# Kernel tuning notes

Hardware: AMD Instinct MI355X
Metric: run time of the kernel (lower is better)

## Reference

```python
import jax, jax.numpy as jnp
import numpy as np

IN_SIZE = 256
HID = 256          # memory_vector_size == hidd_size
MEM = 128          # memory_size
ALPHA_SIG = -0.4
GAMMA = 0.3
GATE = 1.0 / (1.0 + np.exp(-ALPHA_SIG))  # sigmoid(alpha_sig) ~ 0.4013
B, T = 128, 1024


def _l2norm(x):
    # F.normalize(x, dim=-1): x / max(||x||2, 1e-12)
    return x / jnp.maximum(jnp.linalg.norm(x, axis=-1, keepdims=True), 1e-12)


def setup_inputs() -> dict:
    key = jax.random.key(0)
    ks = jax.random.split(key, 5)
    s = 1.0 / np.sqrt(HID)  # torch LSTMCell default init range
    X = jax.random.normal(ks[0], (B, T, IN_SIZE), dtype=jnp.float32)
    W_ih = jax.random.uniform(ks[1], (4 * HID, IN_SIZE), jnp.float32, -s, s)
    W_hh = jax.random.uniform(ks[2], (4 * HID, HID), jnp.float32, -s, s)
    b_ih = jax.random.uniform(ks[3], (4 * HID,), jnp.float32, -s, s)
    b_hh = jax.random.uniform(ks[4], (4 * HID,), jnp.float32, -s, s)
    return {"X": X, "W_ih": W_ih, "W_hh": W_hh, "b_ih": b_ih, "b_hh": b_hh}


def _forward(X, W_ih, W_hh, b_ih, b_hh):
    Bt = X.shape[0]
    gate = jnp.asarray(GATE, X.dtype)
    gamma = jnp.asarray(GAMMA, X.dtype)

    def lstm_cell(x, h, c):
        z = x @ W_ih.T + b_ih + h @ W_hh.T + b_hh  # [B, 4H]
        i, f, g, o = jnp.split(z, 4, axis=-1)
        c_new = jax.nn.sigmoid(f) * c + jax.nn.sigmoid(i) * jnp.tanh(g)
        h_new = jax.nn.sigmoid(o) * jnp.tanh(c_new)
        return h_new, c_new

    def step(carry, x_t):
        h, c, M, w_u, prev_w_r = carry
        h, c = lstm_cell(x_t, h, c)
        # read head: softmax over cosine similarity with memory rows
        inner = h @ M.T                                    # [B, MEM]
        denom = (jnp.linalg.norm(h, axis=-1, keepdims=True)
                 * jnp.linalg.norm(M, axis=-1)[None, :])   # [B, MEM]
        w_r = jax.nn.softmax(inner / (denom + 1e-8), axis=-1)
        read = w_r @ M                                     # [B, H]
        out_t = jnp.concatenate([h, read], axis=-1)        # [B, 2H]
        # write (original is under torch.no_grad / detached)
        hs = jax.lax.stop_gradient(h)
        wrs = jax.lax.stop_gradient(w_r)
        w_lu = (1.0 - gate) * jax.nn.one_hot(jnp.argmin(w_u, axis=-1), MEM, dtype=M.dtype)
        w_w = gate * prev_w_r + w_lu                       # [B, MEM]
        M_new = _l2norm(M + w_w.T @ hs)                    # einsum('bi,bj->bij').sum(0) == w_w.T @ h
        w_u_new = _l2norm(gamma * w_u + wrs + w_w)
        return (h, c, M_new, w_u_new, wrs), out_t

    init = (jnp.zeros((Bt, HID), X.dtype),
            jnp.zeros((Bt, HID), X.dtype),
            jnp.zeros((MEM, HID), X.dtype),   # self.M starts as zeros
            jnp.zeros((Bt, MEM), X.dtype),    # w_u
            jnp.zeros((Bt, MEM), X.dtype))    # prev_w_r
    _, ys = jax.lax.scan(step, init, jnp.swapaxes(X, 0, 1))  # ys: [T, B, 2H]
    return jnp.swapaxes(ys, 0, 1)                            # [B, T, 2H]


def reference(X, W_ih, W_hh, b_ih, b_hh):
    return _forward(X, W_ih, W_hh, b_ih, b_hh)
```

## Files before the change

### kernel.cpp

```cpp
#include <hip/hip_runtime.h>
#include <math.h>

#define BATCH 128
#define TSTEPS 1024
#define INSZ 256
#define HSZ 256
#define MEMN 128

#define NWG_A 128
#define NWG_B 64
#define NWG_C 32
#define NWG 224
#define NTHR 256

#define GATE_C 0.40131233988754794f
#define OMG_C  (1.0f - GATE_C)
#define GAMMA_C 0.3f

__device__ float g_hT[(size_t)TSTEPS * HSZ * BATCH];
__device__ float g_M [(size_t)TSTEPS * MEMN * HSZ];
__device__ float g_Mn[(size_t)TSTEPS * MEMN];
__device__ float g_ww[(size_t)TSTEPS * BATCH * MEMN];
__device__ float g_c[BATCH * HSZ];
__device__ int g_fA[TSTEPS * NWG_A];
__device__ int g_fB[TSTEPS * NWG_B];
__device__ int g_fC[TSTEPS * NWG_C];

__global__ void reset_ctrl_kernel() {
    const int gt = blockIdx.x * 256 + threadIdx.x, gn = gridDim.x * 256;
    for (int i = gt; i < TSTEPS * NWG_A; i += gn)
        __hip_atomic_store(&g_fA[i], 0, __ATOMIC_RELAXED, __HIP_MEMORY_SCOPE_AGENT);
    for (int i = gt; i < TSTEPS * NWG_B; i += gn)
        __hip_atomic_store(&g_fB[i], 0, __ATOMIC_RELAXED, __HIP_MEMORY_SCOPE_AGENT);
    for (int i = gt; i < TSTEPS * NWG_C; i += gn)
        __hip_atomic_store(&g_fC[i], 0, __ATOMIC_RELAXED, __HIP_MEMORY_SCOPE_AGENT);
}

__device__ __forceinline__ float sigf(float x) { return 1.0f / (1.0f + expf(-x)); }

__device__ __forceinline__ void st_wt(float* p, float v) {
    __hip_atomic_store(p, v, __ATOMIC_RELAXED, __HIP_MEMORY_SCOPE_AGENT);
}
__device__ __forceinline__ void st_flag(int* p, int v) {
    __hip_atomic_store(p, v, __ATOMIC_RELAXED, __HIP_MEMORY_SCOPE_AGENT);
}
__device__ __forceinline__ void wait_vm0() { asm volatile("s_waitcnt vmcnt(0)" ::: "memory"); }

__device__ __forceinline__ void wait_flags(int* f, int n, int want, int lane) {
    int it = 0;
    for (;;) {
        bool ok = true;
        for (int i = lane; i < n; i += 64)
            ok &= (__hip_atomic_load(&f[i], __ATOMIC_RELAXED, __HIP_MEMORY_SCOPE_AGENT) == want);
        if (__all(ok)) break;
        __builtin_amdgcn_s_sleep(1);
        if (++it > (1 << 22)) break;
    }
}

__global__ void __launch_bounds__(NTHR, 1)
mann_persist(const float* __restrict__ X, const float* __restrict__ Wih,
             const float* __restrict__ Whh, const float* __restrict__ bih,
             const float* __restrict__ bhh, float* __restrict__ out) {
    __shared__ float4 s_x4[64 * 128];
    __shared__ float s_aux[4096];
    __shared__ float s_red8[8];
    __shared__ unsigned long long s_redu8[8];

    const int w = blockIdx.x, tid = threadIdx.x;
    const int lane = tid & 63, wv = tid >> 6;

    auto red256sum = [&](float v) -> float {
#pragma unroll
        for (int o = 32; o; o >>= 1) v += __shfl_xor(v, o, 64);
        if (lane == 0) s_red8[wv] = v;
        __syncthreads();
        float r = (s_red8[0] + s_red8[1]) + (s_red8[2] + s_red8[3]);
        __syncthreads();
        return r;
    };
    auto grpsum = [&](float v) -> float {
#pragma unroll
        for (int o = 32; o; o >>= 1) v += __shfl_xor(v, o, 64);
        if (lane == 0) s_red8[wv] = v;
        __syncthreads();
        float r = s_red8[(tid >> 7) * 2] + s_red8[(tid >> 7) * 2 + 1];
        __syncthreads();
        return r;
    };
    auto grpmax = [&](float v) -> float {
#pragma unroll
        for (int o = 32; o; o >>= 1) v = fmaxf(v, __shfl_xor(v, o, 64));
        if (lane == 0) s_red8[wv] = v;
        __syncthreads();
        float r = fmaxf(s_red8[(tid >> 7) * 2], s_red8[(tid >> 7) * 2 + 1]);
        __syncthreads();
        return r;
    };
    auto grpminu = [&](unsigned long long v) -> unsigned long long {
#pragma unroll
        for (int o = 32; o; o >>= 1) {
            unsigned long long o2 = __shfl_xor(v, o, 64);
            v = (o2 < v) ? o2 : v;
        }
        if (lane == 0) s_redu8[wv] = v;
        __syncthreads();
        unsigned long long a = s_redu8[(tid >> 7) * 2], b2 = s_redu8[(tid >> 7) * 2 + 1];
        unsigned long long r = (a < b2) ? a : b2;
        __syncthreads();
        return r;
    };

    if (w < NWG_A) {
        const int bb = w >> 6, jb = w & 63;
        const int bglob = bb * 64 + lane;
        float biasA[4];
#pragma unroll
        for (int g = 0; g < 4; ++g) {
            const int row = g * HSZ + jb * 4 + wv;
            biasA[g] = bih[row] + bhh[row];
        }

        auto stageX = [&](int t) {
            const int kq = tid & 63, bofs = tid >> 6;
#pragma unroll 4
            for (int rep = 0; rep < 16; ++rep) {
                const int b = rep * 4 + bofs;
                const float4 v = *(const float4*)(X + ((size_t)(bb * 64 + b) * TSTEPS + t) * INSZ + kq * 4);
                s_x4[b * 128 + (kq ^ (b & 7))] = v;
            }
        };
        auto computeRegion = [&](float (&acc)[16], const float* __restrict__ Wb, const int kofs) {
            const int kbase = kofs + wv * 64;
#pragma unroll 4
            for (int k4 = 0; k4 < 16; ++k4) {
                const int kg = kbase + k4 * 4;
                const float4 xv = s_x4[lane * 128 + ((kg >> 2) ^ (lane & 7))];
                const int kl = kg - kofs;
#pragma unroll
                for (int rr = 0; rr < 16; ++rr) {
                    const int grow = (rr >> 2) * HSZ + jb * 4 + (rr & 3);
                    const float4 wv4 = *(const float4*)(Wb + (size_t)grow * 256 + kl);
                    acc[rr] += wv4.x * xv.x + wv4.y * xv.y + wv4.z * xv.z + wv4.w * xv.w;
                }
            }
        };

        stageX(0);
        __syncthreads();

        for (int t = 0; t < TSTEPS; ++t) {
            float acc[16];
#pragma unroll
            for (int i = 0; i < 16; ++i) acc[i] = 0.f;
            float4 hv[16];
            if (t > 0) {
                if (wv == 0) wait_flags(g_fA + (size_t)(t - 1) * NWG_A, NWG_A, t, lane);
                __syncthreads();
                asm volatile("" ::: "memory");
#pragma unroll
                for (int rep = 0; rep < 16; ++rep) {
                    const int j0 = (wv * 16 + rep) * 4;
                    const size_t base = ((size_t)(t - 1) * HSZ + j0) * BATCH + bglob;
                    float4 v;
                    v.x = g_hT[base];
                    v.y = g_hT[base + BATCH];
                    v.z = g_hT[base + 2 * BATCH];
                    v.w = g_hT[base + 3 * BATCH];
                    hv[rep] = v;
                }
            }
            computeRegion(acc, Wih, 0);
            if (t > 0) {
#pragma unroll
                for (int rep = 0; rep < 16; ++rep)
                    s_x4[lane * 128 + ((64 + wv * 16 + rep) ^ (lane & 7))] = hv[rep];
            } else {
                const float4 z4 = make_float4(0.f, 0.f, 0.f, 0.f);
#pragma unroll
                for (int rep = 0; rep < 16; ++rep)
                    s_x4[lane * 128 + ((64 + wv * 16 + rep) ^ (lane & 7))] = z4;
            }
            __syncthreads();
            computeRegion(acc, Whh, 256);
#pragma unroll
            for (int rr = 0; rr < 16; ++rr) s_aux[(wv * 16 + rr) * 64 + lane] = acc[rr];
            __syncthreads();
            float z[4];
#pragma unroll
            for (int g = 0; g < 4; ++g) {
                const int rr = g * 4 + wv;
                z[g] = ((s_aux[rr * 64 + lane] + s_aux[(16 + rr) * 64 + lane]) +
                        (s_aux[(32 + rr) * 64 + lane] + s_aux[(48 + rr) * 64 + lane])) + biasA[g];
            }
            const int jglob = jb * 4 + wv;
            const int cidx = bglob * HSZ + jglob;
            const float cold = (t == 0) ? 0.f : g_c[cidx];
            const float cn = sigf(z[1]) * cold + sigf(z[0]) * tanhf(z[2]);
            const float hn = sigf(z[3]) * tanhf(cn);
            g_c[cidx] = cn;
            st_wt(&g_hT[((size_t)t * HSZ + jglob) * BATCH + bglob], hn);
            wait_vm0();
            __syncthreads();
            if (tid == 0) st_flag(&g_fA[(size_t)t * NWG_A + w], t + 1);
            if (t + 1 < TSTEPS) stageX(t + 1);
        }
    } else if (w < NWG_A + NWG_B) {
        const int bwg = w - NWG_A;
        const int grp = tid >> 7, lm = tid & 127;
        const int bB = bwg * 2 + grp;
        float* s_h2 = s_aux;
        float* s_wr2 = s_aux + 512;
        float wwreg = (lm == 0) ? OMG_C : 0.f;
        float wureg = 0.f;

        for (int t = 0; t < TSTEPS; ++t) {
            if (wv == 0) wait_flags(g_fA + (size_t)t * NWG_A, NWG_A, t + 1, lane);
            else if (wv == 1 && t > 0) wait_flags(g_fC + (size_t)(t - 1) * NWG_C, NWG_C, t, lane);
            __syncthreads();
            asm volatile("" ::: "memory");
            s_h2[grp * 256 + lm] = g_hT[((size_t)t * HSZ + lm) * BATCH + bB];
            s_h2[grp * 256 + lm + 128] = g_hT[((size_t)t * HSZ + lm + 128) * BATCH + bB];
            __syncthreads();
            const float hv0 = s_h2[grp * 256 + lm], hv1 = s_h2[grp * 256 + lm + 128];
            const float hnorm = sqrtf(grpsum(hv0 * hv0 + hv1 * hv1));
            float sc = 0.f;
            if (t > 0) {
                const float4* mrow = (const float4*)&g_M[((size_t)t * MEMN + lm) * HSZ];
                const float4* h4 = (const float4*)&s_h2[grp * 256];
                float a = 0.f;
#pragma unroll 8
                for (int c = 0; c < 64; ++c) {
                    const float4 m4 = mrow[c], x4 = h4[c];
                    a += m4.x * x4.x + m4.y * x4.y + m4.z * x4.z + m4.w * x4.w;
                }
                const float mn = g_Mn[(size_t)t * MEMN + lm];
                sc = a / (hnorm * mn + 1e-8f);
            }
            const float mx = grpmax(sc);
            const float ev = expf(sc - mx);
            const float es = grpsum(ev);
            const float wr = ev / es;
            s_wr2[grp * 128 + lm] = wr;
            __syncthreads();
            float rd0 = 0.f, rd1 = 0.f;
            if (t > 0) {
#pragma unroll 8
                for (int m = 0; m < 128; ++m) {
                    const float mv = g_M[((size_t)t * MEMN + m) * HSZ + tid];
                    rd0 += s_wr2[m] * mv;
                    rd1 += s_wr2[128 + m] * mv;
                }
            }
            const int b0 = bwg * 2, b1 = b0 + 1;
            float* o0 = out + ((size_t)b0 * TSTEPS + t) * 512;
            float* o1 = out + ((size_t)b1 * TSTEPS + t) * 512;
            o0[tid] = s_h2[tid];
            o1[tid] = s_h2[256 + tid];
            o0[256 + tid] = rd0;
            o1[256 + tid] = rd1;
            const float un = GAMMA_C * wureg + wr + wwreg;
            const float un2 = grpsum(un * un);
            const float us = 1.0f / fmaxf(sqrtf(un2), 1e-12f);
            const float wun = un * us;
            wureg = wun;
            unsigned long long key =
                (((unsigned long long)__float_as_uint(wun)) << 32) | (unsigned)lm;
            const unsigned long long mk = grpminu(key);
            const int amin = (int)(mk & 0xffffffffu);
            const float wwn = GATE_C * wr + ((lm == amin) ? OMG_C : 0.f);
            wwreg = wwn;
            if (t + 1 < TSTEPS)
                st_wt(&g_ww[((size_t)(t + 1) * BATCH + bB) * MEMN + lm], wwn);
            wait_vm0();
            __syncthreads();
            if (tid == 0) st_flag(&g_fB[(size_t)t * NWG_B + bwg], t + 1);
        }
    } else {
        const int cwg = w - NWG_A - NWG_B;
        const int m0 = cwg * 4;
        float* s_wwc = s_aux;

        for (int t = 0; t < TSTEPS - 1; ++t) {
            if (wv == 0) wait_flags(g_fA + (size_t)t * NWG_A, NWG_A, t + 1, lane);
            else if (wv == 1 && t > 0) wait_flags(g_fB + (size_t)(t - 1) * NWG_B, NWG_B, t, lane);
            __syncthreads();
            asm volatile("" ::: "memory");
#pragma unroll
            for (int e = tid; e < 512; e += 256) {
                const int mi = e & 3, b = e >> 2;
                float v;
                if (t > 0) v = g_ww[((size_t)t * BATCH + b) * MEMN + m0 + mi];
                else v = (m0 + mi == 0) ? OMG_C : 0.f;
                s_wwc[mi * 128 + b] = v;
            }
            __syncthreads();
            float macc[4];
#pragma unroll
            for (int mi = 0; mi < 4; ++mi)
                macc[mi] = (t > 0) ? g_M[((size_t)t * MEMN + m0 + mi) * HSZ + tid] : 0.f;
            const float4* ht4 = (const float4*)&g_hT[((size_t)t * HSZ + tid) * BATCH];
#pragma unroll 4
            for (int b4 = 0; b4 < 32; ++b4) {
                const float4 hv4 = ht4[b4];
#pragma unroll
                for (int mi = 0; mi < 4; ++mi) {
                    const float* wc = &s_wwc[mi * 128 + b4 * 4];
                    macc[mi] += wc[0] * hv4.x + wc[1] * hv4.y + wc[2] * hv4.z + wc[3] * hv4.w;
                }
            }
#pragma unroll
            for (int mi = 0; mi < 4; ++mi) {
                const float nrm = sqrtf(red256sum(macc[mi] * macc[mi]));
                const float scale = 1.0f / fmaxf(nrm, 1e-12f);
                const float vo = macc[mi] * scale;
                st_wt(&g_M[((size_t)(t + 1) * MEMN + m0 + mi) * HSZ + tid], vo);
                if (tid == 0) st_wt(&g_Mn[(size_t)(t + 1) * MEMN + m0 + mi], nrm * scale);
            }
            wait_vm0();
            __syncthreads();
            if (tid == 0) st_flag(&g_fC[(size_t)t * NWG_C + cwg], t + 1);
        }
    }
}

extern "C" void kernel_launch(void* const* d_in, const int* in_sizes, int n_in,
                              void* d_out, int out_size, void* d_ws, size_t ws_size,
                              hipStream_t stream) {
    const float* X   = (const float*)d_in[0];
    const float* Wih = (const float*)d_in[1];
    const float* Whh = (const float*)d_in[2];
    const float* bih = (const float*)d_in[3];
    const float* bhh = (const float*)d_in[4];
    float* out = (float*)d_out;
    (void)in_sizes; (void)n_in; (void)out_size; (void)d_ws; (void)ws_size;

    hipLaunchKernelGGL(reset_ctrl_kernel, dim3(224), dim3(256), 0, stream);
    hipLaunchKernelGGL(mann_persist, dim3(NWG), dim3(NTHR), 0, stream,
                       X, Wih, Whh, bih, bhh, out);
}
```

Measured before the change: 24.04 ms.

## Repartition LSTM workgroups by hidden unit with LDS-resident weights and batch-major h copy

The LSTM-stage workgroups now each own two hidden units across the whole batch instead of four units for half the batch. This lets their slice of W_ih/W_hh be cached in LDS once rather than re-read from global memory every timestep, and X and h are staged in double-buffered 128-wide tiles. The cell state stays in a register instead of going to global memory. A batch-major copy of h is also written so the read-head stage gets coalesced loads, and the memory-update stage keeps its M rows in registers. In exchange every LSTM group now stages the full X row for all 128 batches each step, adds extra barriers, and writes h twice.

```diff
diff --git a/kernel.cpp b/kernel.cpp
--- a/kernel.cpp
+++ b/kernel.cpp
@@ -18,10 +18,10 @@
 #define GAMMA_C 0.3f
 
 __device__ float g_hT[(size_t)TSTEPS * HSZ * BATCH];
+__device__ float g_hB[(size_t)TSTEPS * BATCH * HSZ];
 __device__ float g_M [(size_t)TSTEPS * MEMN * HSZ];
 __device__ float g_Mn[(size_t)TSTEPS * MEMN];
 __device__ float g_ww[(size_t)TSTEPS * BATCH * MEMN];
-__device__ float g_c[BATCH * HSZ];
 __device__ int g_fA[TSTEPS * NWG_A];
 __device__ int g_fB[TSTEPS * NWG_B];
 __device__ int g_fC[TSTEPS * NWG_C];
@@ -40,6 +40,11 @@
 
 __device__ __forceinline__ void st_wt(float* p, float v) {
     __hip_atomic_store(p, v, __ATOMIC_RELAXED, __HIP_MEMORY_SCOPE_AGENT);
+}
+__device__ __forceinline__ void st_wt2(float* p, float lo, float hi) {
+    unsigned long long pk = (unsigned long long)__float_as_uint(lo) |
+                            ((unsigned long long)__float_as_uint(hi) << 32);
+    __hip_atomic_store((unsigned long long*)p, pk, __ATOMIC_RELAXED, __HIP_MEMORY_SCOPE_AGENT);
 }
 __device__ __forceinline__ void st_flag(int* p, int v) {
     __hip_atomic_store(p, v, __ATOMIC_RELAXED, __HIP_MEMORY_SCOPE_AGENT);
@@ -62,13 +67,15 @@
 mann_persist(const float* __restrict__ X, const float* __restrict__ Wih,
              const float* __restrict__ Whh, const float* __restrict__ bih,
              const float* __restrict__ bhh, float* __restrict__ out) {
-    __shared__ float4 s_x4[64 * 128];
-    __shared__ float s_aux[4096];
+    __shared__ float4 s_xt[2][4096];
+    __shared__ float4 s_w[1024];
+    __shared__ float s_tr[256];
     __shared__ float s_red8[8];
     __shared__ unsigned long long s_redu8[8];
 
     const int w = blockIdx.x, tid = threadIdx.x;
     const int lane = tid & 63, wv = tid >> 6;
+    float* s_aux = (float*)s_xt;
 
     auto red256sum = [&](float v) -> float {
 #pragma unroll
@@ -112,98 +119,106 @@
     };
 
     if (w < NWG_A) {
-        const int bb = w >> 6, jb = w & 63;
-        const int bglob = bb * 64 + lane;
+        const int j2 = wv >> 1, bh = wv & 1;
+        const int bA = bh * 64 + lane;
+        const int jA = 2 * w + j2;
         float biasA[4];
 #pragma unroll
-        for (int g = 0; g < 4; ++g) {
-            const int row = g * HSZ + jb * 4 + wv;
-            biasA[g] = bih[row] + bhh[row];
-        }
-
-        auto stageX = [&](int t) {
-            const int kq = tid & 63, bofs = tid >> 6;
-#pragma unroll 4
+        for (int g = 0; g < 4; ++g) biasA[g] = bih[g * HSZ + jA] + bhh[g * HSZ + jA];
+
+#pragma unroll
+        for (int rep = 0; rep < 4; ++rep) {
+            const int id = rep * 256 + tid;
+            const int r = id >> 7, c = id & 127;
+            const int grow = (r >> 1) * HSZ + 2 * w + (r & 1);
+            float4 v;
+            if (c < 64) v = ((const float4*)(Wih + (size_t)grow * INSZ))[c];
+            else        v = ((const float4*)(Whh + (size_t)grow * HSZ))[c - 64];
+            s_w[r * 128 + c] = v;
+        }
+
+        auto stageX = [&](int t, int kt, float4* buf) {
+#pragma unroll
             for (int rep = 0; rep < 16; ++rep) {
-                const int b = rep * 4 + bofs;
-                const float4 v = *(const float4*)(X + ((size_t)(bb * 64 + b) * TSTEPS + t) * INSZ + kq * 4);
-                s_x4[b * 128 + (kq ^ (b & 7))] = v;
+                const int id = rep * 256 + tid;
+                const int b = id >> 5, c = id & 31;
+                buf[b * 32 + (c ^ (b & 7))] =
+                    *(const float4*)(X + ((size_t)b * TSTEPS + t) * INSZ + kt * 128 + c * 4);
             }
         };
-        auto computeRegion = [&](float (&acc)[16], const float* __restrict__ Wb, const int kofs) {
-            const int kbase = kofs + wv * 64;
-#pragma unroll 4
-            for (int k4 = 0; k4 < 16; ++k4) {
-                const int kg = kbase + k4 * 4;
-                const float4 xv = s_x4[lane * 128 + ((kg >> 2) ^ (lane & 7))];
-                const int kl = kg - kofs;
-#pragma unroll
-                for (int rr = 0; rr < 16; ++rr) {
-                    const int grow = (rr >> 2) * HSZ + jb * 4 + (rr & 3);
-                    const float4 wv4 = *(const float4*)(Wb + (size_t)grow * 256 + kl);
-                    acc[rr] += wv4.x * xv.x + wv4.y * xv.y + wv4.z * xv.z + wv4.w * xv.w;
+        auto loadH = [&](int tprev, int jt, float4 (&hvr)[16]) {
+#pragma unroll
+            for (int rep = 0; rep < 16; ++rep) {
+                const int id = rep * 256 + tid;
+                const int b = id >> 5, c = id & 31;
+                hvr[rep] = *(const float4*)(g_hB + ((size_t)tprev * BATCH + b) * HSZ + jt * 128 + c * 4);
+            }
+        };
+        auto writeTile = [&](float4 (&hvr)[16], float4* buf) {
+#pragma unroll
+            for (int rep = 0; rep < 16; ++rep) {
+                const int id = rep * 256 + tid;
+                const int b = id >> 5, c = id & 31;
+                buf[b * 32 + (c ^ (b & 7))] = hvr[rep];
+            }
+        };
+        auto computeTile = [&](const float4* buf, int T, float (&zacc)[4]) {
+#pragma unroll 8
+            for (int c = 0; c < 32; ++c) {
+                const float4 xv = buf[bA * 32 + (c ^ (bA & 7))];
+#pragma unroll
+                for (int g = 0; g < 4; ++g) {
+                    const float4 wv4 = s_w[(g * 2 + j2) * 128 + T * 32 + c];
+                    zacc[g] += wv4.x * xv.x + wv4.y * xv.y + wv4.z * xv.z + wv4.w * xv.w;
                 }
             }
         };
 
-        stageX(0);
-        __syncthreads();
+        stageX(0, 0, s_xt[0]);
+        stageX(0, 1, s_xt[1]);
+        __syncthreads();
+        float creg = 0.f;
 
         for (int t = 0; t < TSTEPS; ++t) {
-            float acc[16];
-#pragma unroll
-            for (int i = 0; i < 16; ++i) acc[i] = 0.f;
-            float4 hv[16];
             if (t > 0) {
                 if (wv == 0) wait_flags(g_fA + (size_t)(t - 1) * NWG_A, NWG_A, t, lane);
                 __syncthreads();
                 asm volatile("" ::: "memory");
-#pragma unroll
-                for (int rep = 0; rep < 16; ++rep) {
-                    const int j0 = (wv * 16 + rep) * 4;
-                    const size_t base = ((size_t)(t - 1) * HSZ + j0) * BATCH + bglob;
-                    float4 v;
-                    v.x = g_hT[base];
-                    v.y = g_hT[base + BATCH];
-                    v.z = g_hT[base + 2 * BATCH];
-                    v.w = g_hT[base + 3 * BATCH];
-                    hv[rep] = v;
-                }
-            }
-            computeRegion(acc, Wih, 0);
-            if (t > 0) {
-#pragma unroll
-                for (int rep = 0; rep < 16; ++rep)
-                    s_x4[lane * 128 + ((64 + wv * 16 + rep) ^ (lane & 7))] = hv[rep];
-            } else {
-                const float4 z4 = make_float4(0.f, 0.f, 0.f, 0.f);
-#pragma unroll
-                for (int rep = 0; rep < 16; ++rep)
-                    s_x4[lane * 128 + ((64 + wv * 16 + rep) ^ (lane & 7))] = z4;
-            }
-            __syncthreads();
-            computeRegion(acc, Whh, 256);
-#pragma unroll
-            for (int rr = 0; rr < 16; ++rr) s_aux[(wv * 16 + rr) * 64 + lane] = acc[rr];
-            __syncthreads();
+            }
+            float zacc[4] = {0.f, 0.f, 0.f, 0.f};
+            float4 hvr[16];
+            if (t > 0) loadH(t - 1, 0, hvr);
+            else { const float4 z4 = make_float4(0.f,0.f,0.f,0.f);
+#pragma unroll
+                   for (int r = 0; r < 16; ++r) hvr[r] = z4; }
+            computeTile(s_xt[0], 0, zacc);
+            __syncthreads();
+            writeTile(hvr, s_xt[0]);
+            if (t > 0) loadH(t - 1, 1, hvr);
+            computeTile(s_xt[1], 1, zacc);
+            __syncthreads();
+            writeTile(hvr, s_xt[1]);
+            computeTile(s_xt[0], 2, zacc);
+            __syncthreads();
+            computeTile(s_xt[1], 3, zacc);
             float z[4];
 #pragma unroll
-            for (int g = 0; g < 4; ++g) {
-                const int rr = g * 4 + wv;
-                z[g] = ((s_aux[rr * 64 + lane] + s_aux[(16 + rr) * 64 + lane]) +
-                        (s_aux[(32 + rr) * 64 + lane] + s_aux[(48 + rr) * 64 + lane])) + biasA[g];
-            }
-            const int jglob = jb * 4 + wv;
-            const int cidx = bglob * HSZ + jglob;
-            const float cold = (t == 0) ? 0.f : g_c[cidx];
-            const float cn = sigf(z[1]) * cold + sigf(z[0]) * tanhf(z[2]);
+            for (int g = 0; g < 4; ++g) z[g] = zacc[g] + biasA[g];
+            const float cn = sigf(z[1]) * creg + sigf(z[0]) * tanhf(z[2]);
             const float hn = sigf(z[3]) * tanhf(cn);
-            g_c[cidx] = cn;
-            st_wt(&g_hT[((size_t)t * HSZ + jglob) * BATCH + bglob], hn);
+            creg = cn;
+            st_wt(&g_hT[((size_t)t * HSZ + jA) * BATCH + bA], hn);
+            s_tr[j2 * 128 + bA] = hn;
+            __syncthreads();
+            if (tid < 128)
+                st_wt2(&g_hB[((size_t)t * BATCH + tid) * HSZ + 2 * w], s_tr[tid], s_tr[128 + tid]);
             wait_vm0();
             __syncthreads();
             if (tid == 0) st_flag(&g_fA[(size_t)t * NWG_A + w], t + 1);
-            if (t + 1 < TSTEPS) stageX(t + 1);
+            if (t + 1 < TSTEPS) {
+                stageX(t + 1, 0, s_xt[0]);
+                stageX(t + 1, 1, s_xt[1]);
+            }
         }
     } else if (w < NWG_A + NWG_B) {
         const int bwg = w - NWG_A;
@@ -219,8 +234,8 @@
             else if (wv == 1 && t > 0) wait_flags(g_fC + (size_t)(t - 1) * NWG_C, NWG_C, t, lane);
             __syncthreads();
             asm volatile("" ::: "memory");
-            s_h2[grp * 256 + lm] = g_hT[((size_t)t * HSZ + lm) * BATCH + bB];
-            s_h2[grp * 256 + lm + 128] = g_hT[((size_t)t * HSZ + lm + 128) * BATCH + bB];
+            s_h2[grp * 256 + lm] = g_hB[((size_t)t * BATCH + bB) * HSZ + lm];
+            s_h2[grp * 256 + 128 + lm] = g_hB[((size_t)t * BATCH + bB) * HSZ + 128 + lm];
             __syncthreads();
             const float hv0 = s_h2[grp * 256 + lm], hv1 = s_h2[grp * 256 + lm + 128];
             const float hnorm = sqrtf(grpsum(hv0 * hv0 + hv1 * hv1));
@@ -280,6 +295,7 @@
         const int cwg = w - NWG_A - NWG_B;
         const int m0 = cwg * 4;
         float* s_wwc = s_aux;
+        float mreg[4] = {0.f, 0.f, 0.f, 0.f};
 
         for (int t = 0; t < TSTEPS - 1; ++t) {
             if (wv == 0) wait_flags(g_fA + (size_t)t * NWG_A, NWG_A, t + 1, lane);
@@ -297,8 +313,7 @@
             __syncthreads();
             float macc[4];
 #pragma unroll
-            for (int mi = 0; mi < 4; ++mi)
-                macc[mi] = (t > 0) ? g_M[((size_t)t * MEMN + m0 + mi) * HSZ + tid] : 0.f;
+            for (int mi = 0; mi < 4; ++mi) macc[mi] = mreg[mi];
             const float4* ht4 = (const float4*)&g_hT[((size_t)t * HSZ + tid) * BATCH];
 #pragma unroll 4
             for (int b4 = 0; b4 < 32; ++b4) {
@@ -314,6 +329,7 @@
                 const float nrm = sqrtf(red256sum(macc[mi] * macc[mi]));
                 const float scale = 1.0f / fmaxf(nrm, 1e-12f);
                 const float vo = macc[mi] * scale;
+                mreg[mi] = vo;
                 st_wt(&g_M[((size_t)(t + 1) * MEMN + m0 + mi) * HSZ + tid], vo);
                 if (tid == 0) st_wt(&g_Mn[(size_t)(t + 1) * MEMN + m0 + mi], nrm * scale);
             }
```

Result: slower. 30.31 ms (+26.0%).

## Stage memory into LDS, keep M rows in registers, overlap waits with loads

Applied to the files above, without the earlier changes.

Group B workgroups copy the full memory matrix M into shared memory once per step and read it from there, using an XOR swizzle to avoid bank conflicts, instead of re-reading global M twice. Group C workgroups keep their own M rows in registers across steps and batch the four norm reductions into one barrier pair. The flag waits are reordered so M and w_w loads happen before waiting on the LSTM group, overlapping dependency latency with the loads. This raises register and LDS pressure and changes the synchronisation order between stages.

```diff
diff --git a/kernel.cpp b/kernel.cpp
--- a/kernel.cpp
+++ b/kernel.cpp
@@ -65,20 +65,12 @@
     __shared__ float4 s_x4[64 * 128];
     __shared__ float s_aux[4096];
     __shared__ float s_red8[8];
+    __shared__ float s_red16[16];
     __shared__ unsigned long long s_redu8[8];
 
     const int w = blockIdx.x, tid = threadIdx.x;
     const int lane = tid & 63, wv = tid >> 6;
 
-    auto red256sum = [&](float v) -> float {
-#pragma unroll
-        for (int o = 32; o; o >>= 1) v += __shfl_xor(v, o, 64);
-        if (lane == 0) s_red8[wv] = v;
-        __syncthreads();
-        float r = (s_red8[0] + s_red8[1]) + (s_red8[2] + s_red8[3]);
-        __syncthreads();
-        return r;
-    };
     auto grpsum = [&](float v) -> float {
 #pragma unroll
         for (int o = 32; o; o >>= 1) v += __shfl_xor(v, o, 64);
@@ -109,6 +101,25 @@
         unsigned long long r = (a < b2) ? a : b2;
         __syncthreads();
         return r;
+    };
+    auto red256sum4 = [&](float v0, float v1, float v2, float v3, float (&r)[4]) {
+#pragma unroll
+        for (int o = 32; o; o >>= 1) {
+            v0 += __shfl_xor(v0, o, 64);
+            v1 += __shfl_xor(v1, o, 64);
+            v2 += __shfl_xor(v2, o, 64);
+            v3 += __shfl_xor(v3, o, 64);
+        }
+        if (lane == 0) {
+            s_red16[wv * 4 + 0] = v0; s_red16[wv * 4 + 1] = v1;
+            s_red16[wv * 4 + 2] = v2; s_red16[wv * 4 + 3] = v3;
+        }
+        __syncthreads();
+#pragma unroll
+        for (int k = 0; k < 4; ++k)
+            r[k] = (s_red16[0 * 4 + k] + s_red16[1 * 4 + k]) +
+                   (s_red16[2 * 4 + k] + s_red16[3 * 4 + k]);
+        __syncthreads();
     };
 
     if (w < NWG_A) {
@@ -209,14 +220,26 @@
         const int bwg = w - NWG_A;
         const int grp = tid >> 7, lm = tid & 127;
         const int bB = bwg * 2 + grp;
+        float* s_M = (float*)s_x4;
         float* s_h2 = s_aux;
         float* s_wr2 = s_aux + 512;
         float wwreg = (lm == 0) ? OMG_C : 0.f;
         float wureg = 0.f;
 
         for (int t = 0; t < TSTEPS; ++t) {
+            if (t > 0) {
+                if (wv == 1) wait_flags(g_fC + (size_t)(t - 1) * NWG_C, NWG_C, t, lane);
+                __syncthreads();
+                asm volatile("" ::: "memory");
+                float4 mt[32];
+                const float4* msrc = (const float4*)&g_M[(size_t)t * MEMN * HSZ];
+#pragma unroll
+                for (int i = 0; i < 32; ++i) mt[i] = msrc[i * 256 + tid];
+                float4* md = (float4*)s_M;
+#pragma unroll
+                for (int i = 0; i < 32; ++i) md[i * 256 + tid] = mt[i];
+            }
             if (wv == 0) wait_flags(g_fA + (size_t)t * NWG_A, NWG_A, t + 1, lane);
-            else if (wv == 1 && t > 0) wait_flags(g_fC + (size_t)(t - 1) * NWG_C, NWG_C, t, lane);
             __syncthreads();
             asm volatile("" ::: "memory");
             s_h2[grp * 256 + lm] = g_hT[((size_t)t * HSZ + lm) * BATCH + bB];
@@ -226,12 +249,14 @@
             const float hnorm = sqrtf(grpsum(hv0 * hv0 + hv1 * hv1));
             float sc = 0.f;
             if (t > 0) {
-                const float4* mrow = (const float4*)&g_M[((size_t)t * MEMN + lm) * HSZ];
+                const float4* mrow = (const float4*)&s_M[(size_t)lm * HSZ];
                 const float4* h4 = (const float4*)&s_h2[grp * 256];
+                const int sw = lm & 7;
                 float a = 0.f;
 #pragma unroll 8
                 for (int c = 0; c < 64; ++c) {
-                    const float4 m4 = mrow[c], x4 = h4[c];
+                    const int ci = c ^ sw;
+                    const float4 m4 = mrow[ci], x4 = h4[ci];
                     a += m4.x * x4.x + m4.y * x4.y + m4.z * x4.z + m4.w * x4.w;
                 }
                 const float mn = g_Mn[(size_t)t * MEMN + lm];
@@ -247,7 +272,7 @@
             if (t > 0) {
 #pragma unroll 8
                 for (int m = 0; m < 128; ++m) {
-                    const float mv = g_M[((size_t)t * MEMN + m) * HSZ + tid];
+                    const float mv = s_M[m * HSZ + tid];
                     rd0 += s_wr2[m] * mv;
                     rd1 += s_wr2[128 + m] * mv;
                 }
@@ -280,40 +305,53 @@
         const int cwg = w - NWG_A - NWG_B;
         const int m0 = cwg * 4;
         float* s_wwc = s_aux;
+        float mreg[4] = {0.f, 0.f, 0.f, 0.f};
 
         for (int t = 0; t < TSTEPS - 1; ++t) {
+            if (wv == 1 && t > 0) wait_flags(g_fB + (size_t)(t - 1) * NWG_B, NWG_B, t, lane);
+            __syncthreads();
+            asm volatile("" ::: "memory");
+            {
+                const int e0 = tid, e1 = tid + 256;
+                float v0, v1;
+                if (t > 0) {
+                    v0 = g_ww[((size_t)t * BATCH + (e0 >> 2)) * MEMN + m0 + (e0 & 3)];
+                    v1 = g_ww[((size_t)t * BATCH + (e1 >> 2)) * MEMN + m0 + (e1 & 3)];
+                } else {
+                    v0 = (m0 + (e0 & 3) == 0) ? OMG_C : 0.f;
+                    v1 = (m0 + (e1 & 3) == 0) ? OMG_C : 0.f;
+                }
+                s_wwc[(e0 & 3) * 128 + (e0 >> 2)] = v0;
+                s_wwc[(e1 & 3) * 128 + (e1 >> 2)] = v1;
+            }
             if (wv == 0) wait_flags(g_fA + (size_t)t * NWG_A, NWG_A, t + 1, lane);
-            else if (wv == 1 && t > 0) wait_flags(g_fB + (size_t)(t - 1) * NWG_B, NWG_B, t, lane);
             __syncthreads();
             asm volatile("" ::: "memory");
-#pragma unroll
-            for (int e = tid; e < 512; e += 256) {
-                const int mi = e & 3, b = e >> 2;
-                float v;
-                if (t > 0) v = g_ww[((size_t)t * BATCH + b) * MEMN + m0 + mi];
-                else v = (m0 + mi == 0) ? OMG_C : 0.f;
-                s_wwc[mi * 128 + b] = v;
-            }
-            __syncthreads();
+            float4 hb[32];
+            const float4* ht4 = (const float4*)&g_hT[((size_t)t * HSZ + tid) * BATCH];
+#pragma unroll
+            for (int q = 0; q < 32; ++q) hb[q] = ht4[q];
             float macc[4];
 #pragma unroll
-            for (int mi = 0; mi < 4; ++mi)
-                macc[mi] = (t > 0) ? g_M[((size_t)t * MEMN + m0 + mi) * HSZ + tid] : 0.f;
-            const float4* ht4 = (const float4*)&g_hT[((size_t)t * HSZ + tid) * BATCH];
-#pragma unroll 4
+            for (int mi = 0; mi < 4; ++mi) macc[mi] = mreg[mi];
+#pragma unroll
             for (int b4 = 0; b4 < 32; ++b4) {
-                const float4 hv4 = ht4[b4];
+                const float4 hv4 = hb[b4];
 #pragma unroll
                 for (int mi = 0; mi < 4; ++mi) {
                     const float* wc = &s_wwc[mi * 128 + b4 * 4];
                     macc[mi] += wc[0] * hv4.x + wc[1] * hv4.y + wc[2] * hv4.z + wc[3] * hv4.w;
                 }
             }
+            float nr[4];
+            red256sum4(macc[0] * macc[0], macc[1] * macc[1],
+                       macc[2] * macc[2], macc[3] * macc[3], nr);
 #pragma unroll
             for (int mi = 0; mi < 4; ++mi) {
-                const float nrm = sqrtf(red256sum(macc[mi] * macc[mi]));
+                const float nrm = sqrtf(nr[mi]);
                 const float scale = 1.0f / fmaxf(nrm, 1e-12f);
                 const float vo = macc[mi] * scale;
+                mreg[mi] = vo;
                 st_wt(&g_M[((size_t)(t + 1) * MEMN + m0 + mi) * HSZ + tid], vo);
                 if (tid == 0) st_wt(&g_Mn[(size_t)(t + 1) * MEMN + m0 + mi], nrm * scale);
             }
```

Result: slower. 24.68 ms (+2.6%).
